# Kernel tuning notes

Measured on AMD Instinct MI355X. Metric: run time of the kernel, lower is better.

The kernel has to match this reference:

```python
import jax, jax.numpy as jnp
import numpy as np


def setup_inputs() -> dict:
    key = jax.random.key(0)
    T, B, D, R = 1024, 32, 1024, 256
    ks = jax.random.split(key, 6)
    scale = 1.0 / np.sqrt(D)
    x = jax.random.normal(ks[0], (T, B, D), dtype=jnp.float32)
    h0 = jnp.zeros((B, D), dtype=jnp.float32)
    W_alpha = jax.random.normal(ks[1], (D, D), dtype=jnp.float32) * scale
    b_alpha = jnp.full((D,), 2.0, dtype=jnp.float32)  # init_alpha_bias
    U = jax.random.normal(ks[2], (D, R), dtype=jnp.float32) * (0.5 / np.sqrt(R))
    V = jax.random.normal(ks[3], (R, D), dtype=jnp.float32) * (0.5 * scale)
    W_x = jax.random.normal(ks[4], (D, D), dtype=jnp.float32) * scale
    b = jnp.zeros((D,), dtype=jnp.float32)
    return {"x": x, "h0": h0, "W_alpha": W_alpha, "b_alpha": b_alpha,
            "U": U, "V": V, "W_x": W_x, "b": b}


def reference(x, h0, W_alpha, b_alpha, U, V, W_x, b):
    # Precompute input projections for all timesteps (as in the torch fallback)
    alpha_x_all = jnp.einsum('tbd,ed->tbe', x, W_alpha) + b_alpha  # [T,B,D]
    Wx_all = jnp.einsum('tbd,ed->tbe', x, W_x) + b                 # [T,B,D]

    def step(h_prev, inp):
        ax, wx = inp
        alpha = jax.nn.sigmoid(ax)                       # retain gate
        v = jnp.tanh((h_prev @ V.T) @ U.T + wx)          # low-rank h mixing
        h_new = alpha * h_prev + (1.0 - alpha) * v
        out = h_new * jax.nn.silu(h_new)
        return h_new, (h_new, out)

    _, (h_seq, output) = jax.lax.scan(step, h0, (alpha_x_all, Wx_all))
    h = jnp.concatenate([h0[None], h_seq], axis=0)       # [T+1,B,D]
    return output, h
```

## Files before the change

### kernel.cpp

```cpp
#include <hip/hip_runtime.h>

typedef _Float16 f16;
typedef f16 f16x2 __attribute__((ext_vector_type(2)));
typedef f16 f16x8 __attribute__((ext_vector_type(8)));
typedef float f32x4 __attribute__((ext_vector_type(4)));

#define TT 1024
#define BB 32
#define DD 1024
#define RR 256

__device__ __align__(16) f16 g_VPI[RR * DD];
__device__ __align__(16) f16 g_UPI[DD * RR];

__device__ __forceinline__ float dot2f(f16x2 a, f16x2 b, float c) {
#if __has_builtin(__builtin_amdgcn_fdot2)
    return __builtin_amdgcn_fdot2(a, b, c, false);
#else
    return c + (float)a[0] * (float)b[0] + (float)a[1] * (float)b[1];
#endif
}

__device__ __forceinline__ float sigm_f(float x) { return 1.0f / (1.0f + __expf(-x)); }
__device__ __forceinline__ float tanh_f(float x) { return 1.0f - 2.0f / (1.0f + __expf(2.0f * x)); }

__global__ __launch_bounds__(256)
void fused_pregemm(const float* __restrict__ X, const float* __restrict__ Wa,
                   const float* __restrict__ Wx, const float* __restrict__ ba,
                   const float* __restrict__ bb, f16* __restrict__ axo,
                   f16* __restrict__ wxo)
{
    __shared__ __align__(16) f16 lA[64][40];
    __shared__ __align__(16) f16 lB[64][40];
    __shared__ __align__(16) f16 lC[64][40];

    const int tid = threadIdx.x;
    const int w   = tid >> 6;
    const int l   = tid & 63;
    const int la  = l & 15;
    const int qd  = l >> 4;
    const int m0  = blockIdx.x * 64;
    const int n0  = blockIdx.y * 64;
    const int sr  = tid >> 2;
    const int sk  = (tid & 3) * 8;

    f32x4 accA[4] = {};
    f32x4 accX[4] = {};

    for (int k0 = 0; k0 < DD; k0 += 32) {
        {
            const float* pX = X + (size_t)(m0 + sr) * DD + k0 + sk;
            float4 v0 = *(const float4*)pX;
            float4 v1 = *(const float4*)(pX + 4);
            f16x8 x8 = {(f16)v0.x, (f16)v0.y, (f16)v0.z, (f16)v0.w,
                        (f16)v1.x, (f16)v1.y, (f16)v1.z, (f16)v1.w};
            *(f16x8*)&lA[sr][sk] = x8;

            const float* pA = Wa + (size_t)(n0 + sr) * DD + k0 + sk;
            v0 = *(const float4*)pA;
            v1 = *(const float4*)(pA + 4);
            f16x8 a8 = {(f16)v0.x, (f16)v0.y, (f16)v0.z, (f16)v0.w,
                        (f16)v1.x, (f16)v1.y, (f16)v1.z, (f16)v1.w};
            *(f16x8*)&lB[sr][sk] = a8;

            const float* pW = Wx + (size_t)(n0 + sr) * DD + k0 + sk;
            v0 = *(const float4*)pW;
            v1 = *(const float4*)(pW + 4);
            f16x8 w8 = {(f16)v0.x, (f16)v0.y, (f16)v0.z, (f16)v0.w,
                        (f16)v1.x, (f16)v1.y, (f16)v1.z, (f16)v1.w};
            *(f16x8*)&lC[sr][sk] = w8;
        }
        __syncthreads();

        f16x8 af = *(const f16x8*)&lA[16 * w + la][qd * 8];
        #pragma unroll
        for (int c = 0; c < 4; c++) {
            f16x8 b1 = *(const f16x8*)&lB[16 * c + la][qd * 8];
            f16x8 b2 = *(const f16x8*)&lC[16 * c + la][qd * 8];
            accA[c] = __builtin_amdgcn_mfma_f32_16x16x32_f16(af, b1, accA[c], 0, 0, 0);
            accX[c] = __builtin_amdgcn_mfma_f32_16x16x32_f16(af, b2, accX[c], 0, 0, 0);
        }
        __syncthreads();
    }

    #pragma unroll
    for (int c = 0; c < 4; c++) {
        const int n = n0 + 16 * c + la;
        const float bav = ba[n];
        const float bbv = bb[n];
        #pragma unroll
        for (int r = 0; r < 4; r++) {
            const int m = m0 + 16 * w + qd * 4 + r;
            axo[(size_t)m * DD + n] = (f16)(accA[c][r] + bav);
            wxo[(size_t)m * DD + n] = (f16)(accX[c][r] + bbv);
        }
    }
}

__global__ __launch_bounds__(1024)
void pack_weights(const float* __restrict__ V, const float* __restrict__ U)
{
    const int i   = blockIdx.x;
    const int tid = threadIdx.x;
    const int r   = tid >> 2;
    const int s2  = tid & 3;
    const int j   = (i + s2) & 31;

    const float* sv = V + (size_t)r * DD + 256 * s2 + 8 * j;
    f16x8 v8;
    #pragma unroll
    for (int k = 0; k < 8; k++) v8[k] = (f16)sv[k];
    ((f16x8*)g_VPI)[i * 1024 + tid] = v8;

    const float* su = U + (size_t)tid * RR + 8 * i;
    f16x8 u8;
    #pragma unroll
    for (int k = 0; k < 8; k++) u8[k] = (f16)su[k];
    ((f16x8*)g_UPI)[i * 1024 + tid] = u8;
}

__global__ __launch_bounds__(1024, 4)
void rnn_scan(const f16* __restrict__ ax, const f16* __restrict__ wx,
              const float* __restrict__ h0, float* __restrict__ out,
              float* __restrict__ hout)
{
    const int b   = blockIdx.x;
    const int tid = threadIdx.x;
    const int s2  = tid & 3;
    const int q2  = tid >> 2;

    __shared__ __align__(16) f16 h2[DD];
    __shared__ __align__(16) f16 pl[RR];

    const f16x8* vp  = (const f16x8*)g_VPI + tid;
    const f16x8* up  = (const f16x8*)g_UPI + tid;
    const f16x8* hch = (const f16x8*)h2;
    const f16x8* pch = (const f16x8*)pl;

    const float h0v = h0[(size_t)b * DD + tid];
    float hreg = h0v;
    h2[tid] = (f16)h0v;
    hout[(size_t)b * DD + tid] = h0v;

    const f16* axp   = ax  + (size_t)b * DD + tid;
    const f16* wxp   = wx  + (size_t)b * DD + tid;
    float*     outp  = out + (size_t)b * DD + tid;
    float*     houtp = hout + (size_t)BB * DD + (size_t)b * DD + tid;

    __syncthreads();

    #pragma unroll 1
    for (int t = 0; t < TT; t++) {
        const float axv = (float)*axp;
        const float wxv = (float)*wxp;

        float a0 = 0.f, a1 = 0.f, a2 = 0.f, a3 = 0.f;
        #pragma unroll
        for (int i = 0; i < 32; i++) {
            f16x8 w  = vp[(size_t)i << 10];
            f16x8 hv = hch[32 * s2 + ((i + s2) & 31)];
            f16x2 w0 = {w[0],  w[1]},  w1 = {w[2],  w[3]};
            f16x2 w2 = {w[4],  w[5]},  w3 = {w[6],  w[7]};
            f16x2 p0 = {hv[0], hv[1]}, p1 = {hv[2], hv[3]};
            f16x2 p2 = {hv[4], hv[5]}, p3 = {hv[6], hv[7]};
            a0 = dot2f(w0, p0, a0);
            a1 = dot2f(w1, p1, a1);
            a2 = dot2f(w2, p2, a2);
            a3 = dot2f(w3, p3, a3);
        }
        float p = (a0 + a1) + (a2 + a3);
        p += __shfl_xor(p, 1);
        p += __shfl_xor(p, 2);
        if (s2 == 0) pl[q2] = (f16)p;
        __syncthreads();

        float u0 = 0.f, u1 = 0.f, u2 = 0.f, u3 = 0.f;
        #pragma unroll
        for (int i = 0; i < 32; i++) {
            f16x8 w  = up[(size_t)i << 10];
            f16x8 pv = pch[i];
            f16x2 w0 = {w[0],  w[1]},  w1 = {w[2],  w[3]};
            f16x2 w2 = {w[4],  w[5]},  w3 = {w[6],  w[7]};
            f16x2 q0 = {pv[0], pv[1]}, q1 = {pv[2], pv[3]};
            f16x2 q2v = {pv[4], pv[5]}, q3 = {pv[6], pv[7]};
            u0 = dot2f(w0, q0, u0);
            u1 = dot2f(w1, q1, u1);
            u2 = dot2f(w2, q2v, u2);
            u3 = dot2f(w3, q3, u3);
        }

        const float uu = (u0 + u1) + (u2 + u3) + wxv;
        const float vv = tanh_f(uu);
        const float aa = sigm_f(axv);
        const float hn = aa * hreg + (1.0f - aa) * vv;
        const float so = hn * hn * sigm_f(hn);
        *outp  = so;
        *houtp = hn;
        hreg = hn;
        h2[tid] = (f16)hn;
        axp += BB * DD; wxp += BB * DD; outp += BB * DD; houtp += BB * DD;
        __syncthreads();
    }
}

extern "C" void kernel_launch(void* const* d_in, const int* in_sizes, int n_in,
                              void* d_out, int out_size, void* d_ws, size_t ws_size,
                              hipStream_t stream) {
    (void)in_sizes; (void)n_in; (void)out_size; (void)ws_size;
    const float* x  = (const float*)d_in[0];
    const float* h0 = (const float*)d_in[1];
    const float* Wa = (const float*)d_in[2];
    const float* ba = (const float*)d_in[3];
    const float* U  = (const float*)d_in[4];
    const float* V  = (const float*)d_in[5];
    const float* Wx = (const float*)d_in[6];
    const float* bb = (const float*)d_in[7];

    float* out  = (float*)d_out;
    float* hout = out + (size_t)TT * BB * DD;

    f16* ax16 = (f16*)d_ws;
    f16* wx16 = ax16 + (size_t)TT * BB * DD;

    pack_weights<<<dim3(32), dim3(1024), 0, stream>>>(V, U);
    dim3 g1(512, 16);
    fused_pregemm<<<g1, dim3(256), 0, stream>>>(x, Wa, Wx, ba, bb, ax16, wx16);
    rnn_scan<<<dim3(BB), dim3(1024), 0, stream>>>(ax16, wx16, h0, out, hout);
}
```

Before: 14.01 ms.

## Software-pipeline weight loads across scan stages with repacked wider per-thread tiles

New measurement: 24.59 ms. 75.5% more time.

```diff
diff --git a/kernel.cpp b/kernel.cpp
--- a/kernel.cpp
+++ b/kernel.cpp
@@ -10,8 +10,8 @@
 #define DD 1024
 #define RR 256
 
-__device__ __align__(16) f16 g_VPI[RR * DD];
-__device__ __align__(16) f16 g_UPI[DD * RR];
+__device__ __align__(16) f16 g_VP2[16 * 1024 * 16];
+__device__ __align__(16) f16 g_UP4[8 * 1024 * 32];
 
 __device__ __forceinline__ float dot2f(f16x2 a, f16x2 b, float c) {
 #if __has_builtin(__builtin_amdgcn_fdot2)
@@ -23,6 +23,12 @@
 
 __device__ __forceinline__ float sigm_f(float x) { return 1.0f / (1.0f + __expf(-x)); }
 __device__ __forceinline__ float tanh_f(float x) { return 1.0f - 2.0f / (1.0f + __expf(2.0f * x)); }
+
+__device__ __forceinline__ void wg_barrier() {
+    asm volatile("s_waitcnt lgkmcnt(0)" ::: "memory");
+    __builtin_amdgcn_s_barrier();
+    asm volatile("" ::: "memory");
+}
 
 __global__ __launch_bounds__(256)
 void fused_pregemm(const float* __restrict__ X, const float* __restrict__ Wa,
@@ -100,23 +106,110 @@
 __global__ __launch_bounds__(1024)
 void pack_weights(const float* __restrict__ V, const float* __restrict__ U)
 {
-    const int i   = blockIdx.x;
-    const int tid = threadIdx.x;
-    const int r   = tid >> 2;
-    const int s2  = tid & 3;
-    const int j   = (i + s2) & 31;
-
-    const float* sv = V + (size_t)r * DD + 256 * s2 + 8 * j;
-    f16x8 v8;
-    #pragma unroll
-    for (int k = 0; k < 8; k++) v8[k] = (f16)sv[k];
-    ((f16x8*)g_VPI)[i * 1024 + tid] = v8;
-
-    const float* su = U + (size_t)tid * RR + 8 * i;
-    f16x8 u8;
-    #pragma unroll
-    for (int k = 0; k < 8; k++) u8[k] = (f16)su[k];
-    ((f16x8*)g_UPI)[i * 1024 + tid] = u8;
+    const int j = blockIdx.x;
+    const int t = threadIdx.x;
+    {
+        const int q3 = t >> 3, s3 = t & 7;
+        const int c  = 16 * s3 + ((j + s3) & 15);
+        const float* s0 = V + (size_t)(2 * q3)     * DD + 8 * c;
+        const float* s1 = V + (size_t)(2 * q3 + 1) * DD + 8 * c;
+        f16x8 a, bvec;
+        #pragma unroll
+        for (int k = 0; k < 8; k++) { a[k] = (f16)s0[k]; bvec[k] = (f16)s1[k]; }
+        f16x8* dst = (f16x8*)g_VP2 + ((size_t)j * 1024 + t) * 2;
+        dst[0] = a; dst[1] = bvec;
+    }
+    if (j < 8) {
+        const int q = t >> 2, z4 = t & 3;
+        const int c2 = 8 * z4 + ((j + z4) & 7);
+        f16x8* dst = (f16x8*)g_UP4 + ((size_t)j * 1024 + t) * 4;
+        #pragma unroll
+        for (int k = 0; k < 4; k++) {
+            const float* su = U + (size_t)(4 * q + k) * RR + 8 * c2;
+            f16x8 u8;
+            #pragma unroll
+            for (int m = 0; m < 8; m++) u8[m] = (f16)su[m];
+            dst[k] = u8;
+        }
+    }
+}
+
+template<int S>
+__device__ __forceinline__ void issue_s1(f16x8* buf, const f16x8* vW, int tid) {
+    #pragma unroll
+    for (int k = 0; k < 4; k++) {
+        unsigned idx = ((unsigned)(4 * S + k) << 10) + (unsigned)tid;
+        buf[2 * k]     = vW[idx * 2u];
+        buf[2 * k + 1] = vW[idx * 2u + 1u];
+    }
+}
+
+template<int S>
+__device__ __forceinline__ void comp_s1(const f16x8* buf, const f16x8* hch, int s3,
+                                        float& aA0, float& aA1, float& aB0, float& aB1) {
+    #pragma unroll
+    for (int k = 0; k < 4; k++) {
+        const int j = 4 * S + k;
+        f16x8 hv = hch[16 * s3 + ((j + s3) & 15)];
+        f16x8 wA = buf[2 * k], wB = buf[2 * k + 1];
+        f16x2 h0 = {hv[0], hv[1]}, h1 = {hv[2], hv[3]};
+        f16x2 h2v = {hv[4], hv[5]}, h3 = {hv[6], hv[7]};
+        f16x2 t0 = {wA[0], wA[1]}, t1 = {wA[2], wA[3]};
+        f16x2 t2 = {wA[4], wA[5]}, t3 = {wA[6], wA[7]};
+        aA0 = dot2f(t0, h0, aA0);  aA1 = dot2f(t1, h1, aA1);
+        aA0 = dot2f(t2, h2v, aA0); aA1 = dot2f(t3, h3, aA1);
+        f16x2 r0 = {wB[0], wB[1]}, r1 = {wB[2], wB[3]};
+        f16x2 r2 = {wB[4], wB[5]}, r3 = {wB[6], wB[7]};
+        aB0 = dot2f(r0, h0, aB0);  aB1 = dot2f(r1, h1, aB1);
+        aB0 = dot2f(r2, h2v, aB0); aB1 = dot2f(r3, h3, aB1);
+    }
+}
+
+template<int S>
+__device__ __forceinline__ void issue_s2(f16x8* buf, const f16x8* uW, int tid) {
+    #pragma unroll
+    for (int k = 0; k < 2; k++) {
+        unsigned idx = ((unsigned)(2 * S + k) << 10) + (unsigned)tid;
+        #pragma unroll
+        for (int m = 0; m < 4; m++)
+            buf[4 * k + m] = uW[idx * 4u + (unsigned)m];
+    }
+}
+
+template<int S>
+__device__ __forceinline__ void comp_s2(const f16x8* buf, const f16x8* pch, int z4,
+                                        float& u0, float& u1, float& u2, float& u3) {
+    #pragma unroll
+    for (int k = 0; k < 2; k++) {
+        const int j = 2 * S + k;
+        f16x8 pv = pch[8 * z4 + ((j + z4) & 7)];
+        f16x2 p0 = {pv[0], pv[1]}, p1 = {pv[2], pv[3]};
+        f16x2 p2 = {pv[4], pv[5]}, p3 = {pv[6], pv[7]};
+        {
+            f16x8 w = buf[4 * k + 0];
+            f16x2 w0 = {w[0], w[1]}, w1 = {w[2], w[3]}, w2 = {w[4], w[5]}, w3 = {w[6], w[7]};
+            u0 = dot2f(w0, p0, u0); u0 = dot2f(w1, p1, u0);
+            u0 = dot2f(w2, p2, u0); u0 = dot2f(w3, p3, u0);
+        }
+        {
+            f16x8 w = buf[4 * k + 1];
+            f16x2 w0 = {w[0], w[1]}, w1 = {w[2], w[3]}, w2 = {w[4], w[5]}, w3 = {w[6], w[7]};
+            u1 = dot2f(w0, p0, u1); u1 = dot2f(w1, p1, u1);
+            u1 = dot2f(w2, p2, u1); u1 = dot2f(w3, p3, u1);
+        }
+        {
+            f16x8 w = buf[4 * k + 2];
+            f16x2 w0 = {w[0], w[1]}, w1 = {w[2], w[3]}, w2 = {w[4], w[5]}, w3 = {w[6], w[7]};
+            u2 = dot2f(w0, p0, u2); u2 = dot2f(w1, p1, u2);
+            u2 = dot2f(w2, p2, u2); u2 = dot2f(w3, p3, u2);
+        }
+        {
+            f16x8 w = buf[4 * k + 3];
+            f16x2 w0 = {w[0], w[1]}, w1 = {w[2], w[3]}, w2 = {w[4], w[5]}, w3 = {w[6], w[7]};
+            u3 = dot2f(w0, p0, u3); u3 = dot2f(w1, p1, u3);
+            u3 = dot2f(w2, p2, u3); u3 = dot2f(w3, p3, u3);
+        }
+    }
 }
 
 __global__ __launch_bounds__(1024, 4)
@@ -126,14 +219,15 @@
 {
     const int b   = blockIdx.x;
     const int tid = threadIdx.x;
-    const int s2  = tid & 3;
-    const int q2  = tid >> 2;
+    const int s3  = tid & 7;
+    const int q3  = tid >> 3;
+    const int z4  = tid & 3;
 
     __shared__ __align__(16) f16 h2[DD];
-    __shared__ __align__(16) f16 pl[RR];
-
-    const f16x8* vp  = (const f16x8*)g_VPI + tid;
-    const f16x8* up  = (const f16x8*)g_UPI + tid;
+    __shared__ __align__(4)  f16 pl[RR];
+
+    const f16x8* vW  = (const f16x8*)g_VP2;
+    const f16x8* uW  = (const f16x8*)g_UP4;
     const f16x8* hch = (const f16x8*)h2;
     const f16x8* pch = (const f16x8*)pl;
 
@@ -147,49 +241,45 @@
     float*     outp  = out + (size_t)b * DD + tid;
     float*     houtp = hout + (size_t)BB * DD + (size_t)b * DD + tid;
 
-    __syncthreads();
+    f16x8 bufA[8], bufB[8];
+
+    issue_s1<0>(bufA, vW, tid);
+    issue_s1<1>(bufB, vW, tid);
+    wg_barrier();
 
     #pragma unroll 1
     for (int t = 0; t < TT; t++) {
         const float axv = (float)*axp;
         const float wxv = (float)*wxp;
 
-        float a0 = 0.f, a1 = 0.f, a2 = 0.f, a3 = 0.f;
-        #pragma unroll
-        for (int i = 0; i < 32; i++) {
-            f16x8 w  = vp[(size_t)i << 10];
-            f16x8 hv = hch[32 * s2 + ((i + s2) & 31)];
-            f16x2 w0 = {w[0],  w[1]},  w1 = {w[2],  w[3]};
-            f16x2 w2 = {w[4],  w[5]},  w3 = {w[6],  w[7]};
-            f16x2 p0 = {hv[0], hv[1]}, p1 = {hv[2], hv[3]};
-            f16x2 p2 = {hv[4], hv[5]}, p3 = {hv[6], hv[7]};
-            a0 = dot2f(w0, p0, a0);
-            a1 = dot2f(w1, p1, a1);
-            a2 = dot2f(w2, p2, a2);
-            a3 = dot2f(w3, p3, a3);
-        }
-        float p = (a0 + a1) + (a2 + a3);
-        p += __shfl_xor(p, 1);
-        p += __shfl_xor(p, 2);
-        if (s2 == 0) pl[q2] = (f16)p;
-        __syncthreads();
+        float aA0 = 0.f, aA1 = 0.f, aB0 = 0.f, aB1 = 0.f;
+        comp_s1<0>(bufA, hch, s3, aA0, aA1, aB0, aB1);  issue_s1<2>(bufA, vW, tid);
+        comp_s1<1>(bufB, hch, s3, aA0, aA1, aB0, aB1);  issue_s1<3>(bufB, vW, tid);
+        comp_s1<2>(bufA, hch, s3, aA0, aA1, aB0, aB1);  issue_s2<0>(bufA, uW, tid);
+        comp_s1<3>(bufB, hch, s3, aA0, aA1, aB0, aB1);  issue_s2<1>(bufB, uW, tid);
+
+        float pA = aA0 + aA1, pB = aB0 + aB1;
+        pA += __shfl_xor(pA, 1); pA += __shfl_xor(pA, 2); pA += __shfl_xor(pA, 4);
+        pB += __shfl_xor(pB, 1); pB += __shfl_xor(pB, 2); pB += __shfl_xor(pB, 4);
+        if (s3 == 0) {
+            f16x2 pp; pp[0] = (f16)pA; pp[1] = (f16)pB;
+            *(f16x2*)&pl[2 * q3] = pp;
+        }
+        wg_barrier();
 
         float u0 = 0.f, u1 = 0.f, u2 = 0.f, u3 = 0.f;
-        #pragma unroll
-        for (int i = 0; i < 32; i++) {
-            f16x8 w  = up[(size_t)i << 10];
-            f16x8 pv = pch[i];
-            f16x2 w0 = {w[0],  w[1]},  w1 = {w[2],  w[3]};
-            f16x2 w2 = {w[4],  w[5]},  w3 = {w[6],  w[7]};
-            f16x2 q0 = {pv[0], pv[1]}, q1 = {pv[2], pv[3]};
-            f16x2 q2v = {pv[4], pv[5]}, q3 = {pv[6], pv[7]};
-            u0 = dot2f(w0, q0, u0);
-            u1 = dot2f(w1, q1, u1);
-            u2 = dot2f(w2, q2v, u2);
-            u3 = dot2f(w3, q3, u3);
-        }
-
-        const float uu = (u0 + u1) + (u2 + u3) + wxv;
+        comp_s2<0>(bufA, pch, z4, u0, u1, u2, u3);  issue_s2<2>(bufA, uW, tid);
+        comp_s2<1>(bufB, pch, z4, u0, u1, u2, u3);  issue_s2<3>(bufB, uW, tid);
+        comp_s2<2>(bufA, pch, z4, u0, u1, u2, u3);  issue_s1<0>(bufA, vW, tid);
+        comp_s2<3>(bufB, pch, z4, u0, u1, u2, u3);  issue_s1<1>(bufB, vW, tid);
+
+        u0 += __shfl_xor(u0, 1); u1 += __shfl_xor(u1, 1);
+        u2 += __shfl_xor(u2, 1); u3 += __shfl_xor(u3, 1);
+        u0 += __shfl_xor(u0, 2); u1 += __shfl_xor(u1, 2);
+        u2 += __shfl_xor(u2, 2); u3 += __shfl_xor(u3, 2);
+        float uu = (z4 == 0) ? u0 : (z4 == 1) ? u1 : (z4 == 2) ? u2 : u3;
+
+        uu += wxv;
         const float vv = tanh_f(uu);
         const float aa = sigm_f(axv);
         const float hn = aa * hreg + (1.0f - aa) * vv;
@@ -199,7 +289,7 @@
         hreg = hn;
         h2[tid] = (f16)hn;
         axp += BB * DD; wxp += BB * DD; outp += BB * DD; houtp += BB * DD;
-        __syncthreads();
+        wg_barrier();
     }
 }
 
@@ -222,7 +312,7 @@
     f16* ax16 = (f16*)d_ws;
     f16* wx16 = ax16 + (size_t)TT * BB * DD;
 
-    pack_weights<<<dim3(32), dim3(1024), 0, stream>>>(V, U);
+    pack_weights<<<dim3(16), dim3(1024), 0, stream>>>(V, U);
     dim3 g1(512, 16);
     fused_pregemm<<<g1, dim3(256), 0, stream>>>(x, Wa, Wx, ba, bb, ax16, wx16);
     rnn_scan<<<dim3(BB), dim3(1024), 0, stream>>>(ax16, wx16, h0, out, hout);
```
